# Optimization experiments

Hardware: AMD Instinct MI355X
Metric: run time of the kernel (lower is better)

Reference implementation:

```python
import jax, jax.numpy as jnp
import numpy as np

N_VARS = 28
HID = 64
BATCH = 32768
BN_EPS = 1e-5


def _lin_init(key, fan_in, shape):
    bound = 1.0 / np.sqrt(fan_in)
    return jax.random.uniform(key, shape, minval=-bound, maxval=bound, dtype=jnp.float32)


def setup_inputs() -> dict:
    key = jax.random.key(0)
    ks = jax.random.split(key, 8)
    n, h = N_VARS, HID
    X = jax.random.normal(ks[0], (BATCH, n), dtype=jnp.float32)
    W_logits = jax.random.uniform(ks[1], (n, n), minval=-0.01, maxval=0.01, dtype=jnp.float32)
    # per-mechanism (grouped) weights, stacked on leading mechanism axis n
    W1 = _lin_init(ks[2], n, (n, h, n)); b1 = _lin_init(ks[3], n, (n, h))
    W2 = _lin_init(ks[4], h, (n, h, h)); b2 = _lin_init(ks[5], h, (n, h))
    W3 = _lin_init(ks[6], h, (n, 1, h)); b3 = _lin_init(ks[7], h, (n, 1))
    gamma1 = jnp.ones((n, h)); beta1 = jnp.zeros((n, h))
    gamma2 = jnp.ones((n, h)); beta2 = jnp.zeros((n, h))
    return {"X": X, "W_logits": W_logits,
            "W1": W1, "b1": b1, "gamma1": gamma1, "beta1": beta1,
            "W2": W2, "b2": b2, "gamma2": gamma2, "beta2": beta2,
            "W3": W3, "b3": b3}


def _bn(x, gamma, beta):
    # x: [n, B, h]; batch stats over B (training-mode BatchNorm1d, biased var)
    m = x.mean(axis=1, keepdims=True)
    v = ((x - m) ** 2).mean(axis=1, keepdims=True)
    return gamma[:, None, :] * (x - m) * jax.lax.rsqrt(v + BN_EPS) + beta[:, None, :]


def reference(X, W_logits, W1, b1, gamma1, beta1, W2, b2, gamma2, beta2, W3, b3):
    n = W_logits.shape[0]
    # adjacency: sigmoid with zeroed diagonal
    W = jax.nn.sigmoid(W_logits) * (1.0 - jnp.eye(n, dtype=W_logits.dtype))
    # fuse the parent mask into the first layer's weights: one grouped GEMM
    # instead of n_vars separate masked matmuls
    W1_eff = W1 * W[:, None, :]                               # [n, h, n]
    h1 = jnp.einsum('bd,nhd->nbh', X, W1_eff) + b1[:, None, :]  # [n, B, h]
    a1 = jax.nn.gelu(_bn(h1, gamma1, beta1), approximate=False)
    h2 = jnp.einsum('nbh,ngh->nbg', a1, W2) + b2[:, None, :]
    a2 = jax.nn.gelu(_bn(h2, gamma2, beta2), approximate=False)
    out = jnp.einsum('nbh,noh->nbo', a2, W3) + b3[:, None, :]   # [n, B, 1]
    X_hat = out[:, :, 0].T                                     # [B, n]
    return (X_hat, W)
```

## Files before the change

kernel.cpp:

```cpp
#include <hip/hip_runtime.h>
#include <hip/hip_bf16.h>
#include <math.h>

typedef float  f4 __attribute__((ext_vector_type(4)));
typedef short  s8 __attribute__((ext_vector_type(8)));
typedef int    i2 __attribute__((ext_vector_type(2)));

#define NV 28
#define NB 32768
#define BN_EPS 1e-5f
#define NSLOT 434
#define PBLK 64

#define SUM2_OFF   0
#define SSQ2_OFF   1792
#define GATE_OFF   5376
#define PART_OFF   9472
#define BF_BASE_F  120640
#define XBF_OFF_S  172032
#define H2_BYTE_OFF 2924544ull
#define H2_BYTES    117440512ull

#define SMEM_BYTES 35840

__device__ __forceinline__ float gelu_f(float x) {
    float x2 = x * x;
    float z  = x * __builtin_fmaf(x2, -0.10294324f, -2.3022082f);
    float t  = __builtin_amdgcn_exp2f(z);
    return x * __builtin_amdgcn_rcpf(1.0f + t);
}
__device__ __forceinline__ unsigned short f2bf(float x) {
    unsigned u = __builtin_bit_cast(unsigned, x);
    return (unsigned short)((u + 0x7fffu + ((u >> 16) & 1u)) >> 16);
}
__device__ __forceinline__ int bfpack(float a, float b) {
    unsigned ua = __builtin_bit_cast(unsigned, a) + 0x8000u;
    unsigned ub = __builtin_bit_cast(unsigned, b) + 0x8000u;
    return __builtin_amdgcn_perm(ub, ua, 0x07060302);
}
__device__ __forceinline__ float row16_sum(float v) {
    int x;
    x = __builtin_amdgcn_update_dpp(0, __builtin_bit_cast(int, v), 0xB1, 0xF, 0xF, true);
    v += __builtin_bit_cast(float, x);
    x = __builtin_amdgcn_update_dpp(0, __builtin_bit_cast(int, v), 0x4E, 0xF, 0xF, true);
    v += __builtin_bit_cast(float, x);
    x = __builtin_amdgcn_update_dpp(0, __builtin_bit_cast(int, v), 0x124, 0xF, 0xF, true);
    v += __builtin_bit_cast(float, x);
    x = __builtin_amdgcn_update_dpp(0, __builtin_bit_cast(int, v), 0x128, 0xF, 0xF, true);
    v += __builtin_bit_cast(float, x);
    return v;
}
__device__ __forceinline__ float quad4_sum(float v) {
    int x;
    x = __builtin_amdgcn_update_dpp(0, __builtin_bit_cast(int, v), 0xB1, 0xF, 0xF, true);
    v += __builtin_bit_cast(float, x);
    x = __builtin_amdgcn_update_dpp(0, __builtin_bit_cast(int, v), 0x4E, 0xF, 0xF, true);
    v += __builtin_bit_cast(float, x);
    return v;
}
__device__ __forceinline__ void slot_de(int s, int& d, int& e) {
    int p = s - 28, dd = 0, rem = 28;
    while (p >= rem) { p -= rem; ++dd; --rem; }
    d = dd; e = dd + p;
}

__global__ __launch_bounds__(256) void k_prep(const float* __restrict__ X,
                                              const float* __restrict__ Wlog,
                                              float* __restrict__ ws,
                                              float* __restrict__ out) {
    __shared__ float sx[128 * 28];
    const int b = blockIdx.x, tid = threadIdx.x;
    if (b == PBLK) {
        for (int i = tid; i < 3584; i += 256) ws[SUM2_OFF + i] = 0.0f;
        unsigned* gates = (unsigned*)(ws + GATE_OFF);
        for (int i = tid; i < 28 * 32; i += 256) gates[i] = 0u;
        for (int i = tid; i < 784; i += 256) {
            float w = 1.0f / (1.0f + expf(-Wlog[i]));
            if ((i / 28) == (i % 28)) w = 0.0f;
            out[917504 + i] = w;
        }
        return;
    }
    const int s0 = tid;
    int d0 = 0, e0 = 0;
    if (s0 >= 28) slot_de(s0, d0, e0);
    const int s1 = tid + 256;
    const bool h1v = (s1 < NSLOT);
    int d1 = 0, e1 = 0;
    if (h1v) slot_de(s1, d1, e1);

    float a0 = 0.0f, a1 = 0.0f;
    int* xb = (int*)((short*)(ws + BF_BASE_F) + XBF_OFF_S);
#pragma unroll 1
    for (int ss = 0; ss < 4; ++ss) {
        const int rowbase = b * 512 + ss * 128;
        __syncthreads();
        {
            const f4* src = (const f4*)(X + (size_t)rowbase * 28);
            f4* dst = (f4*)sx;
            for (int i = tid; i < 896; i += 256) dst[i] = src[i];
        }
        __syncthreads();
        for (int j = tid; j < 2048; j += 256) {
            int row = j >> 4, cc = j & 15;
            float lo = (2 * cc     < 28) ? sx[row * 28 + 2 * cc]     : 0.0f;
            float hi = (2 * cc + 1 < 28) ? sx[row * 28 + 2 * cc + 1] : 0.0f;
            xb[(size_t)(rowbase + row) * 16 + cc] = (int)f2bf(lo) | ((int)f2bf(hi) << 16);
        }
        if (s0 < 28) {
            for (int r = 0; r < 128; ++r) a0 += sx[r * 28 + s0];
        } else {
            for (int r = 0; r < 128; ++r)
                a0 = __builtin_fmaf(sx[r * 28 + d0], sx[r * 28 + e0], a0);
        }
        if (h1v) {
            for (int r = 0; r < 128; ++r)
                a1 = __builtin_fmaf(sx[r * 28 + d1], sx[r * 28 + e1], a1);
        }
    }
    ws[PART_OFF + b * NSLOT + s0] = a0;
    if (h1v) ws[PART_OFF + b * NSLOT + s1] = a1;
}

__device__ __forceinline__ void fold_local(char* smemc, const float* __restrict__ Wlog,
                                           const float* __restrict__ W1,
                                           const float* __restrict__ g1,
                                           const float* __restrict__ be1,
                                           const float* __restrict__ W2,
                                           const float* __restrict__ ws, int n) {
    short* sW1   = (short*)smemc;
    short* sW2   = (short*)(smemc + 5120);
    float* fb    = (float*)(smemc + 14336);
    float* sstat = fb;
    float* mu    = fb + 434;
    float* wrow  = fb + 462;
    float* C     = fb + 490;
    float* w1e_s = fb + 1274;
    float* sBias = (float*)(smemc + 34816);
    const int t = threadIdx.x;

    __syncthreads();
    for (int s = t; s < NSLOT; s += 256) {
        float a = 0.0f;
#pragma unroll 8
        for (int p = 0; p < PBLK; ++p) a += ws[PART_OFF + p * NSLOT + s];
        sstat[s] = a;
    }
#pragma unroll
    for (int k = 0; k < 2; ++k) {
        int i = t + k * 256;
        int r = i >> 3, c = i & 7;
        const float* src = W2 + (size_t)n * 4096 + r * 64 + c * 8;
        s8 pk;
#pragma unroll
        for (int j = 0; j < 8; ++j) pk[j] = (short)f2bf(src[j]);
        *(s8*)&sW2[r * 72 + c * 8] = pk;
    }
    __syncthreads();
    if (t < 28) {
        mu[t] = sstat[t] * (1.0f / 32768.0f);
        float w = 1.0f / (1.0f + expf(-Wlog[n * 28 + t]));
        if (t == n) w = 0.0f;
        wrow[t] = w;
    }
    __syncthreads();
    for (int i = t; i < 784; i += 256) {
        int d = i / 28, e = i % 28;
        int lo = d < e ? d : e, hi = d < e ? e : d;
        int idx = 28 + lo * 28 - (lo * (lo - 1)) / 2 + (hi - lo);
        C[i] = sstat[idx] * (1.0f / 32768.0f) - mu[d] * mu[e];
    }
    for (int i = t; i < 1792; i += 256)
        w1e_s[i] = W1[(size_t)n * 1792 + i] * wrow[i % 28];
    __syncthreads();

    const int h = t >> 2, j = t & 3;
    const float* we = &w1e_s[h * 28];
    float var_p = 0.0f, dot_p = 0.0f;
#pragma unroll
    for (int k = 0; k < 7; ++k) {
        int d = 7 * j + k;
        float inner = 0.0f;
#pragma unroll
        for (int e = 0; e < 28; ++e) inner = __builtin_fmaf(C[d * 28 + e], we[e], inner);
        float wd = we[d];
        var_p = __builtin_fmaf(inner, wd, var_p);
        dot_p = __builtin_fmaf(wd, mu[d], dot_p);
    }
    float var  = quad4_sum(var_p);
    float dotm = quad4_sum(dot_p);
    float scale = g1[n * 64 + h] * rsqrtf(fmaxf(var, 0.0f) + BN_EPS);
    if (j == 0) sBias[h] = be1[n * 64 + h] - dotm * scale;
    {
        s8 pk;
#pragma unroll
        for (int k = 0; k < 8; ++k) {
            int d = 8 * j + k;
            pk[k] = (short)f2bf(d < 28 ? we[d] * scale : 0.0f);
        }
        *(s8*)&sW1[h * 40 + 8 * j] = pk;
    }
    __syncthreads();
}

__device__ __forceinline__ void pass1_item(char* smemc, float* __restrict__ ws,
                                           short* __restrict__ h2buf, int item) {
    short* sW1 = (short*)smemc;
    short* sW2 = (short*)(smemc + 5120);
    short* sA1 = (short*)(smemc + 14336);
    float* sP1 = (float*)(smemc + 32768);
    float* sP2 = (float*)(smemc + 33792);
    float* sBias = (float*)(smemc + 34816);
    const int n = item >> 8;
    const int blk = item & 255;
    const int tid = threadIdx.x;
    const int wave = tid >> 6;
    const int lane = tid & 63;
    const int m = lane & 15;
    const int q = lane >> 4;

    const short* xbf = (const short*)(ws + BF_BASE_F) + XBF_OFF_S;

    __syncthreads();
    f4 biasv[4];
#pragma unroll
    for (int t = 0; t < 4; ++t) biasv[t] = *(const f4*)&sBias[16 * t + 4 * q];

    short* myA1a = &sA1[(wave * 2 + 0) * 16 * 72];
    short* myA1b = &sA1[(wave * 2 + 1) * 16 * 72];
    float s1[16], s2v[16];

    const int row0 = blk * 128 + wave * 32;
    s8 xfa = *(const s8*)&xbf[(size_t)(row0 + m) * 32 + 8 * q];
    s8 xfb = *(const s8*)&xbf[(size_t)(row0 + 16 + m) * 32 + 8 * q];

    f4 acc1a[4], acc1b[4];
#pragma unroll
    for (int t = 0; t < 4; ++t) {
        s8 wf = *(const s8*)&sW1[(16 * t + m) * 40 + q * 8];
        acc1a[t] = __builtin_amdgcn_mfma_f32_16x16x32_bf16(wf, xfa, (f4){0.f, 0.f, 0.f, 0.f}, 0, 0, 0);
        acc1b[t] = __builtin_amdgcn_mfma_f32_16x16x32_bf16(wf, xfb, (f4){0.f, 0.f, 0.f, 0.f}, 0, 0, 0);
    }
#pragma unroll
    for (int t = 0; t < 4; ++t) {
        float ga0 = gelu_f(acc1a[t][0] + biasv[t][0]);
        float ga1 = gelu_f(acc1a[t][1] + biasv[t][1]);
        float ga2 = gelu_f(acc1a[t][2] + biasv[t][2]);
        float ga3 = gelu_f(acc1a[t][3] + biasv[t][3]);
        float gb0 = gelu_f(acc1b[t][0] + biasv[t][0]);
        float gb1 = gelu_f(acc1b[t][1] + biasv[t][1]);
        float gb2 = gelu_f(acc1b[t][2] + biasv[t][2]);
        float gb3 = gelu_f(acc1b[t][3] + biasv[t][3]);
        i2 pa = (i2){bfpack(ga0, ga1), bfpack(ga2, ga3)};
        i2 pb = (i2){bfpack(gb0, gb1), bfpack(gb2, gb3)};
        *(i2*)&myA1a[m * 72 + 16 * t + 4 * q] = pa;
        *(i2*)&myA1b[m * 72 + 16 * t + 4 * q] = pb;
    }
    s8 af0a = *(const s8*)&myA1a[m * 72 + 8 * q];
    s8 af1a = *(const s8*)&myA1a[m * 72 + 32 + 8 * q];
    s8 af0b = *(const s8*)&myA1b[m * 72 + 8 * q];
    s8 af1b = *(const s8*)&myA1b[m * 72 + 32 + 8 * q];
    short* hpA = h2buf + ((size_t)n * NB + row0 + m) * 64;
    short* hpB = h2buf + ((size_t)n * NB + row0 + 16 + m) * 64;
#pragma unroll
    for (int u = 0; u < 4; ++u) {
        s8 w0 = *(const s8*)&sW2[(16 * u + m) * 72 + 8 * q];
        s8 w1 = *(const s8*)&sW2[(16 * u + m) * 72 + 32 + 8 * q];
        f4 aa = (f4){0.f, 0.f, 0.f, 0.f};
        f4 ab = (f4){0.f, 0.f, 0.f, 0.f};
        aa = __builtin_amdgcn_mfma_f32_16x16x32_bf16(w0, af0a, aa, 0, 0, 0);
        ab = __builtin_amdgcn_mfma_f32_16x16x32_bf16(w0, af0b, ab, 0, 0, 0);
        aa = __builtin_amdgcn_mfma_f32_16x16x32_bf16(w1, af1a, aa, 0, 0, 0);
        ab = __builtin_amdgcn_mfma_f32_16x16x32_bf16(w1, af1b, ab, 0, 0, 0);
        i2 ha = (i2){bfpack(aa[0], aa[1]), bfpack(aa[2], aa[3])};
        i2 hb = (i2){bfpack(ab[0], ab[1]), bfpack(ab[2], ab[3])};
        *(i2*)&hpA[16 * u + 4 * q] = ha;
        *(i2*)&hpB[16 * u + 4 * q] = hb;
#pragma unroll
        for (int r = 0; r < 4; ++r) {
            s1[u * 4 + r]  = aa[r] + ab[r];
            float sq = __builtin_fmaf(aa[r], aa[r], ab[r] * ab[r]);
            s2v[u * 4 + r] = sq;
        }
    }
#pragma unroll
    for (int u = 0; u < 4; ++u) {
#pragma unroll
        for (int r = 0; r < 4; ++r) {
            float t1 = row16_sum(s1[u * 4 + r]);
            float t2 = row16_sum(s2v[u * 4 + r]);
            if (m == 0) {
                sP1[wave * 64 + 16 * u + 4 * q + r] = t1;
                sP2[wave * 64 + 16 * u + 4 * q + r] = t2;
            }
        }
    }
    __syncthreads();
    if (tid < 64) {
        float a = sP1[tid] + sP1[64 + tid] + sP1[128 + tid] + sP1[192 + tid];
        float b = sP2[tid] + sP2[64 + tid] + sP2[128 + tid] + sP2[192 + tid];
        atomicAdd(&ws[SUM2_OFF + n * 64 + tid], a);
        atomicAdd(&ws[SSQ2_OFF + n * 64 + tid], b);
    }
}

template <bool GATED>
__device__ __forceinline__ void pass2_item(char* smemc, const float* __restrict__ g2,
                                           const float* __restrict__ be2,
                                           const float* __restrict__ W3,
                                           const float* __restrict__ b3,
                                           float* __restrict__ ws,
                                           const short* __restrict__ h2buf,
                                           float* __restrict__ out, int item,
                                           unsigned* gates) {
    float* sSc  = (float*)(smemc + 35072);
    float* sSh  = (float*)(smemc + 35328);
    float* sW3v = (float*)(smemc + 35584);
    const int n = item >> 8;
    const int rbase = (item & 255) * 128;
    const int tid = threadIdx.x;
    if (GATED && tid == 0) {
        while (__hip_atomic_load(&gates[n * 32], __ATOMIC_RELAXED, __HIP_MEMORY_SCOPE_AGENT) < 256u)
            __builtin_amdgcn_s_sleep(2);
    }
    __syncthreads();
    if (tid < 64) {
        float su, sq;
        if (GATED) {
            su = __hip_atomic_load(&ws[SUM2_OFF + n * 64 + tid], __ATOMIC_RELAXED, __HIP_MEMORY_SCOPE_AGENT);
            sq = __hip_atomic_load(&ws[SSQ2_OFF + n * 64 + tid], __ATOMIC_RELAXED, __HIP_MEMORY_SCOPE_AGENT);
        } else {
            su = ws[SUM2_OFF + n * 64 + tid];
            sq = ws[SSQ2_OFF + n * 64 + tid];
        }
        float mean = su * (1.0f / 32768.0f);
        float var  = sq * (1.0f / 32768.0f) - mean * mean;
        float sc = g2[n * 64 + tid] * rsqrtf(fmaxf(var, 0.0f) + BN_EPS);
        sSc[tid]  = sc;
        sSh[tid]  = be2[n * 64 + tid] - mean * sc;
        sW3v[tid] = W3[n * 64 + tid];
    }
    __syncthreads();
    const int wave = tid >> 6;
    const int lane = tid & 63;
    const int rr = lane >> 3;
    const int cc = lane & 7;
    f4 scA = *(const f4*)&sSc[cc * 8],  scB = *(const f4*)&sSc[cc * 8 + 4];
    f4 shA = *(const f4*)&sSh[cc * 8],  shB = *(const f4*)&sSh[cc * 8 + 4];
    f4 w3A = *(const f4*)&sW3v[cc * 8], w3B = *(const f4*)&sW3v[cc * 8 + 4];
    const float b3n = b3[n];
#pragma unroll
    for (int it = 0; it < 4; ++it) {
        const int row = rbase + wave * 32 + it * 8 + rr;
        s8 hv = *(const s8*)(h2buf + ((size_t)n * NB + row) * 64 + cc * 8);
        float p = 0.0f;
#pragma unroll
        for (int j = 0; j < 4; ++j) {
            float v = __builtin_fmaf(__builtin_bit_cast(float, ((int)(unsigned short)hv[j]) << 16), scA[j], shA[j]);
            p = __builtin_fmaf(gelu_f(v), w3A[j], p);
        }
#pragma unroll
        for (int j = 0; j < 4; ++j) {
            float v = __builtin_fmaf(__builtin_bit_cast(float, ((int)(unsigned short)hv[4 + j]) << 16), scB[j], shB[j]);
            p = __builtin_fmaf(gelu_f(v), w3B[j], p);
        }
        p += __shfl_xor(p, 1);
        p += __shfl_xor(p, 2);
        p += __shfl_xor(p, 4);
        if (cc == 0) out[(size_t)row * 28 + n] = p + b3n;
    }
}

__global__ __launch_bounds__(256, 4) void k_mainG(const float* __restrict__ Wlog,
                                                  const float* __restrict__ W1,
                                                  const float* __restrict__ g1,
                                                  const float* __restrict__ be1,
                                                  const float* __restrict__ W2,
                                                  const float* __restrict__ g2,
                                                  const float* __restrict__ be2,
                                                  const float* __restrict__ W3,
                                                  const float* __restrict__ b3,
                                                  float* __restrict__ ws,
                                                  short* __restrict__ h2buf,
                                                  float* __restrict__ out) {
    __shared__ __align__(16) char smem[SMEM_BYTES];
    unsigned* gates = (unsigned*)(ws + GATE_OFF);
    const int b = blockIdx.x;
    const int tid = threadIdx.x;
    const int i0 = 7 * b;

    int cur = -1;
#pragma unroll 1
    for (int k = 0; k < 7; ++k) {
        const int item = i0 + k;
        const int n = item >> 8;
        if (n != cur) { fold_local(smem, Wlog, W1, g1, be1, W2, ws, n); cur = n; }
        pass1_item(smem, ws, h2buf, item);
        __syncthreads();
        if (tid == 0)
            __hip_atomic_fetch_add(&gates[n * 32], 1u, __ATOMIC_RELAXED, __HIP_MEMORY_SCOPE_AGENT);
    }
#pragma unroll 1
    for (int k = 0; k < 7; ++k)
        pass2_item<true>(smem, g2, be2, W3, b3, ws, h2buf, out, i0 + k, gates);
}

__global__ __launch_bounds__(256, 4) void kf_p1(const float* __restrict__ Wlog,
                                                const float* __restrict__ W1,
                                                const float* __restrict__ g1,
                                                const float* __restrict__ be1,
                                                const float* __restrict__ W2,
                                                float* __restrict__ ws,
                                                short* __restrict__ h2buf) {
    __shared__ __align__(16) char smem[SMEM_BYTES];
    const int i0 = 7 * blockIdx.x;
    int cur = -1;
#pragma unroll 1
    for (int k = 0; k < 7; ++k) {
        const int item = i0 + k;
        const int n = item >> 8;
        if (n != cur) { fold_local(smem, Wlog, W1, g1, be1, W2, ws, n); cur = n; }
        pass1_item(smem, ws, h2buf, item);
    }
}
__global__ __launch_bounds__(256, 4) void kf_p2(const float* __restrict__ g2,
                                                const float* __restrict__ be2,
                                                const float* __restrict__ W3,
                                                const float* __restrict__ b3,
                                                float* __restrict__ ws,
                                                const short* __restrict__ h2buf,
                                                float* __restrict__ out) {
    __shared__ __align__(16) char smem[SMEM_BYTES];
    const int i0 = 7 * blockIdx.x;
#pragma unroll 1
    for (int k = 0; k < 7; ++k)
        pass2_item<false>(smem, g2, be2, W3, b3, ws, h2buf, out, i0 + k, nullptr);
}

extern "C" void kernel_launch(void* const* d_in, const int* in_sizes, int n_in,
                              void* d_out, int out_size, void* d_ws, size_t ws_size,
                              hipStream_t stream) {
    const float* X   = (const float*)d_in[0];
    const float* Wl  = (const float*)d_in[1];
    const float* W1  = (const float*)d_in[2];
    const float* g1  = (const float*)d_in[4];
    const float* be1 = (const float*)d_in[5];
    const float* W2  = (const float*)d_in[6];
    const float* g2  = (const float*)d_in[8];
    const float* be2 = (const float*)d_in[9];
    const float* W3  = (const float*)d_in[10];
    const float* b3  = (const float*)d_in[11];
    float* out = (float*)d_out;
    float* ws  = (float*)d_ws;
    short* h2buf = (short*)((char*)d_ws + H2_BYTE_OFF);

    static int gmain = 0;
    if (gmain == 0) {
        int dev = 0;
        hipDeviceProp_t prop;
        bool ok = (hipGetDevice(&dev) == hipSuccess) &&
                  (hipGetDeviceProperties(&prop, dev) == hipSuccess) &&
                  prop.cooperativeLaunch;
        int bpc = 0;
        if (ok &&
            hipOccupancyMaxActiveBlocksPerMultiprocessor(&bpc, k_mainG, 256, 0) == hipSuccess &&
            (long)bpc * prop.multiProcessorCount >= 1024) {
            gmain = 1;
        } else {
            gmain = -1;
        }
    }

    k_prep<<<dim3(PBLK + 1), dim3(256), 0, stream>>>(X, Wl, ws, out);

    bool done = false;
    if (gmain > 0) {
        void* args[12] = {(void*)&Wl, (void*)&W1, (void*)&g1, (void*)&be1, (void*)&W2,
                          (void*)&g2, (void*)&be2, (void*)&W3, (void*)&b3,
                          (void*)&ws, (void*)&h2buf, (void*)&out};
        hipError_t e = hipLaunchCooperativeKernel(reinterpret_cast<const void*>(k_mainG),
                                                  dim3(1024), dim3(256), args, 0, stream);
        if (e == hipSuccess) done = true;
        else gmain = -1;
    }
    if (!done) {
        kf_p1<<<dim3(1024), dim3(256), 0, stream>>>(Wl, W1, g1, be1, W2, ws, h2buf);
        kf_p2<<<dim3(1024), dim3(256), 0, stream>>>(g2, be2, W3, b3, ws, h2buf, out);
    }
}
```

Baseline: 203.2 us.

## Compute first-layer BN fold once per mechanism and share via global gates

The first-layer weight fold (covariance reduction, BN scale and bias, bf16 packing) used to be recomputed by every block for every mechanism it touched. It now runs once per mechanism in 28 designated blocks, which publish the folded W1 and bias to global memory and set a per-mechanism gate. The remaining blocks spin on that gate and copy the results into shared memory. W2 is converted to bf16 once in extra prep blocks instead of per block. This removes redundant fold work, but every block now has to wait for the 28 folding blocks before starting, which adds a dependency stall.

```diff
diff --git a/kernel.cpp b/kernel.cpp
--- a/kernel.cpp
+++ b/kernel.cpp
@@ -15,8 +15,11 @@
 #define SUM2_OFF   0
 #define SSQ2_OFF   1792
 #define GATE_OFF   5376
-#define PART_OFF   9472
+#define BIAS1_OFF  7424
+#define W1F_OFF    9216
+#define PART_OFF   37888
 #define BF_BASE_F  120640
+#define W2B_OFF_S  57344
 #define XBF_OFF_S  172032
 #define H2_BYTE_OFF 2924544ull
 #define H2_BYTES    117440512ull
@@ -66,6 +69,7 @@
 
 __global__ __launch_bounds__(256) void k_prep(const float* __restrict__ X,
                                               const float* __restrict__ Wlog,
+                                              const float* __restrict__ W2,
                                               float* __restrict__ ws,
                                               float* __restrict__ out) {
     __shared__ float sx[128 * 28];
@@ -73,12 +77,25 @@
     if (b == PBLK) {
         for (int i = tid; i < 3584; i += 256) ws[SUM2_OFF + i] = 0.0f;
         unsigned* gates = (unsigned*)(ws + GATE_OFF);
-        for (int i = tid; i < 28 * 32; i += 256) gates[i] = 0u;
+        for (int i = tid; i < 2048; i += 256) gates[i] = 0u;
         for (int i = tid; i < 784; i += 256) {
             float w = 1.0f / (1.0f + expf(-Wlog[i]));
             if ((i / 28) == (i % 28)) w = 0.0f;
             out[917504 + i] = w;
         }
+        return;
+    }
+    if (b > PBLK) {
+        const int n = b - PBLK - 1;
+        const float* w2src = W2 + (size_t)n * 4096 + tid * 16;
+        short* w2d = (short*)(ws + BF_BASE_F) + W2B_OFF_S + (size_t)n * 4096 + tid * 16;
+        s8 a, c;
+#pragma unroll
+        for (int k = 0; k < 8; ++k) a[k] = (short)f2bf(w2src[k]);
+#pragma unroll
+        for (int k = 0; k < 8; ++k) c[k] = (short)f2bf(w2src[8 + k]);
+        *(s8*)&w2d[0] = a;
+        *(s8*)&w2d[8] = c;
         return;
     }
     const int s0 = tid;
@@ -122,40 +139,25 @@
     if (h1v) ws[PART_OFF + b * NSLOT + s1] = a1;
 }
 
-__device__ __forceinline__ void fold_local(char* smemc, const float* __restrict__ Wlog,
-                                           const float* __restrict__ W1,
-                                           const float* __restrict__ g1,
-                                           const float* __restrict__ be1,
-                                           const float* __restrict__ W2,
-                                           const float* __restrict__ ws, int n) {
-    short* sW1   = (short*)smemc;
-    short* sW2   = (short*)(smemc + 5120);
+__device__ __forceinline__ void fold_global(char* smemc, const float* __restrict__ Wlog,
+                                            const float* __restrict__ W1,
+                                            const float* __restrict__ g1,
+                                            const float* __restrict__ be1,
+                                            float* __restrict__ ws, int n) {
     float* fb    = (float*)(smemc + 14336);
     float* sstat = fb;
     float* mu    = fb + 434;
     float* wrow  = fb + 462;
     float* C     = fb + 490;
     float* w1e_s = fb + 1274;
-    float* sBias = (float*)(smemc + 34816);
     const int t = threadIdx.x;
 
-    __syncthreads();
     for (int s = t; s < NSLOT; s += 256) {
         float a = 0.0f;
 #pragma unroll 8
         for (int p = 0; p < PBLK; ++p) a += ws[PART_OFF + p * NSLOT + s];
         sstat[s] = a;
     }
-#pragma unroll
-    for (int k = 0; k < 2; ++k) {
-        int i = t + k * 256;
-        int r = i >> 3, c = i & 7;
-        const float* src = W2 + (size_t)n * 4096 + r * 64 + c * 8;
-        s8 pk;
-#pragma unroll
-        for (int j = 0; j < 8; ++j) pk[j] = (short)f2bf(src[j]);
-        *(s8*)&sW2[r * 72 + c * 8] = pk;
-    }
     __syncthreads();
     if (t < 28) {
         mu[t] = sstat[t] * (1.0f / 32768.0f);
@@ -190,15 +192,56 @@
     float var  = quad4_sum(var_p);
     float dotm = quad4_sum(dot_p);
     float scale = g1[n * 64 + h] * rsqrtf(fmaxf(var, 0.0f) + BN_EPS);
-    if (j == 0) sBias[h] = be1[n * 64 + h] - dotm * scale;
-    {
-        s8 pk;
-#pragma unroll
-        for (int k = 0; k < 8; ++k) {
-            int d = 8 * j + k;
-            pk[k] = (short)f2bf(d < 28 ? we[d] * scale : 0.0f);
-        }
-        *(s8*)&sW1[h * 40 + 8 * j] = pk;
+    if (j == 0)
+        __hip_atomic_store(&ws[BIAS1_OFF + n * 64 + h], be1[n * 64 + h] - dotm * scale,
+                           __ATOMIC_RELAXED, __HIP_MEMORY_SCOPE_AGENT);
+    unsigned* w1f = (unsigned*)ws + W1F_OFF + n * 1024;
+#pragma unroll
+    for (int k = 0; k < 4; ++k) {
+        int d0 = 8 * j + 2 * k, d1 = d0 + 1;
+        unsigned lo = (unsigned)f2bf(d0 < 28 ? we[d0] * scale : 0.0f);
+        unsigned hi = (unsigned)f2bf(d1 < 28 ? we[d1] * scale : 0.0f);
+        __hip_atomic_store(&w1f[h * 16 + j * 4 + k], lo | (hi << 16),
+                           __ATOMIC_RELAXED, __HIP_MEMORY_SCOPE_AGENT);
+    }
+    __syncthreads();
+    if (t == 0)
+        __hip_atomic_store((unsigned*)(ws + GATE_OFF) + 896 + n * 32, 1u,
+                           __ATOMIC_RELAXED, __HIP_MEMORY_SCOPE_AGENT);
+}
+
+template <bool GATED>
+__device__ __forceinline__ void weights_stage(char* smemc, float* __restrict__ ws, int n) {
+    short* sW1   = (short*)smemc;
+    short* sW2   = (short*)(smemc + 5120);
+    float* sBias = (float*)(smemc + 34816);
+    const int tid = threadIdx.x;
+    __syncthreads();
+    if (GATED && tid == 0) {
+        unsigned* wg = (unsigned*)(ws + GATE_OFF) + 896 + n * 32;
+        while (__hip_atomic_load(wg, __ATOMIC_RELAXED, __HIP_MEMORY_SCOPE_AGENT) < 1u)
+            __builtin_amdgcn_s_sleep(2);
+    }
+    __syncthreads();
+    const unsigned* w1f = (const unsigned*)ws + W1F_OFF + n * 1024;
+#pragma unroll
+    for (int k = 0; k < 4; ++k) {
+        int i = tid + k * 256;
+        unsigned v = GATED ? __hip_atomic_load(&w1f[i], __ATOMIC_RELAXED, __HIP_MEMORY_SCOPE_AGENT)
+                           : w1f[i];
+        int r = i >> 4, c = i & 15;
+        *(unsigned*)((char*)sW1 + r * 80 + c * 4) = v;
+    }
+    if (tid < 64)
+        sBias[tid] = GATED ? __hip_atomic_load(&ws[BIAS1_OFF + n * 64 + tid],
+                                               __ATOMIC_RELAXED, __HIP_MEMORY_SCOPE_AGENT)
+                           : ws[BIAS1_OFF + n * 64 + tid];
+    const short* w2g = (const short*)(ws + BF_BASE_F) + W2B_OFF_S + (size_t)n * 4096;
+#pragma unroll
+    for (int k = 0; k < 2; ++k) {
+        int i = tid + k * 256;
+        int r = i >> 3, c = i & 7;
+        *(s8*)&sW2[r * 72 + c * 8] = *(const s8*)&w2g[r * 64 + c * 8];
     }
     __syncthreads();
 }
@@ -279,8 +322,7 @@
 #pragma unroll
         for (int r = 0; r < 4; ++r) {
             s1[u * 4 + r]  = aa[r] + ab[r];
-            float sq = __builtin_fmaf(aa[r], aa[r], ab[r] * ab[r]);
-            s2v[u * 4 + r] = sq;
+            s2v[u * 4 + r] = __builtin_fmaf(aa[r], aa[r], ab[r] * ab[r]);
         }
     }
 #pragma unroll
@@ -375,7 +417,6 @@
                                                   const float* __restrict__ W1,
                                                   const float* __restrict__ g1,
                                                   const float* __restrict__ be1,
-                                                  const float* __restrict__ W2,
                                                   const float* __restrict__ g2,
                                                   const float* __restrict__ be2,
                                                   const float* __restrict__ W3,
@@ -389,12 +430,14 @@
     const int tid = threadIdx.x;
     const int i0 = 7 * b;
 
+    if (b < 28) fold_global(smem, Wlog, W1, g1, be1, ws, b);
+
     int cur = -1;
 #pragma unroll 1
     for (int k = 0; k < 7; ++k) {
         const int item = i0 + k;
         const int n = item >> 8;
-        if (n != cur) { fold_local(smem, Wlog, W1, g1, be1, W2, ws, n); cur = n; }
+        if (n != cur) { weights_stage<true>(smem, ws, n); cur = n; }
         pass1_item(smem, ws, h2buf, item);
         __syncthreads();
         if (tid == 0)
@@ -405,12 +448,15 @@
         pass2_item<true>(smem, g2, be2, W3, b3, ws, h2buf, out, i0 + k, gates);
 }
 
-__global__ __launch_bounds__(256, 4) void kf_p1(const float* __restrict__ Wlog,
-                                                const float* __restrict__ W1,
-                                                const float* __restrict__ g1,
-                                                const float* __restrict__ be1,
-                                                const float* __restrict__ W2,
-                                                float* __restrict__ ws,
+__global__ __launch_bounds__(256) void kf_fold(const float* __restrict__ Wlog,
+                                               const float* __restrict__ W1,
+                                               const float* __restrict__ g1,
+                                               const float* __restrict__ be1,
+                                               float* __restrict__ ws) {
+    __shared__ __align__(16) char smem[SMEM_BYTES];
+    fold_global(smem, Wlog, W1, g1, be1, ws, blockIdx.x);
+}
+__global__ __launch_bounds__(256, 4) void kf_p1(float* __restrict__ ws,
                                                 short* __restrict__ h2buf) {
     __shared__ __align__(16) char smem[SMEM_BYTES];
     const int i0 = 7 * blockIdx.x;
@@ -419,7 +465,7 @@
     for (int k = 0; k < 7; ++k) {
         const int item = i0 + k;
         const int n = item >> 8;
-        if (n != cur) { fold_local(smem, Wlog, W1, g1, be1, W2, ws, n); cur = n; }
+        if (n != cur) { weights_stage<false>(smem, ws, n); cur = n; }
         pass1_item(smem, ws, h2buf, item);
     }
 }
@@ -471,11 +517,11 @@
         }
     }
 
-    k_prep<<<dim3(PBLK + 1), dim3(256), 0, stream>>>(X, Wl, ws, out);
+    k_prep<<<dim3(PBLK + 1 + 28), dim3(256), 0, stream>>>(X, Wl, W2, ws, out);
 
     bool done = false;
     if (gmain > 0) {
-        void* args[12] = {(void*)&Wl, (void*)&W1, (void*)&g1, (void*)&be1, (void*)&W2,
+        void* args[11] = {(void*)&Wl, (void*)&W1, (void*)&g1, (void*)&be1,
                           (void*)&g2, (void*)&be2, (void*)&W3, (void*)&b3,
                           (void*)&ws, (void*)&h2buf, (void*)&out};
         hipError_t e = hipLaunchCooperativeKernel(reinterpret_cast<const void*>(k_mainG),
@@ -484,7 +530,8 @@
         else gmain = -1;
     }
     if (!done) {
-        kf_p1<<<dim3(1024), dim3(256), 0, stream>>>(Wl, W1, g1, be1, W2, ws, h2buf);
-        kf_p2<<<dim3(1024), dim3(256), 0, stream>>>(g2, be2, W3, b3, ws, h2buf, out);
-    }
-}
+        kf_fold<<<dim3(28),   dim3(256), 0, stream>>>(Wl, W1, g1, be1, ws);
+        kf_p1  <<<dim3(1024), dim3(256), 0, stream>>>(ws, h2buf);
+        kf_p2  <<<dim3(1024), dim3(256), 0, stream>>>(g2, be2, W3, b3, ws, h2buf, out);
+    }
+}
```

Result: faster. 194.7 us (-4.2%).

## Replace cooperative gated kernel with three plain launches and precomputed bf16 W2

Applied to the files above, without the earlier changes.

Removes the cooperative single-kernel path, whose blocks spin on per-mechanism gate counters between pass 1 and pass 2, and replaces it with three ordinary launches: prep, pass 1 and pass 2. Pass 1 now uses 896 blocks, each bound to one mechanism so the BN1 fold runs once per block. Pass 2 becomes a fine-grained kernel with one 128-row tile per block. The bf16 conversion of W2 moves into extra prep blocks so each pass-1 block copies pre-converted weights. This trades the gate spin-waits and the cooperative launch for an extra kernel boundary and more, smaller pass-2 blocks.

```diff
diff --git a/kernel.cpp b/kernel.cpp
--- a/kernel.cpp
+++ b/kernel.cpp
@@ -14,14 +14,14 @@
 
 #define SUM2_OFF   0
 #define SSQ2_OFF   1792
-#define GATE_OFF   5376
 #define PART_OFF   9472
 #define BF_BASE_F  120640
+#define W2B_OFF_S  57344
 #define XBF_OFF_S  172032
 #define H2_BYTE_OFF 2924544ull
 #define H2_BYTES    117440512ull
 
-#define SMEM_BYTES 35840
+#define SMEM_BYTES 35072
 
 __device__ __forceinline__ float gelu_f(float x) {
     float x2 = x * x;
@@ -66,19 +66,31 @@
 
 __global__ __launch_bounds__(256) void k_prep(const float* __restrict__ X,
                                               const float* __restrict__ Wlog,
+                                              const float* __restrict__ W2,
                                               float* __restrict__ ws,
                                               float* __restrict__ out) {
     __shared__ float sx[128 * 28];
     const int b = blockIdx.x, tid = threadIdx.x;
     if (b == PBLK) {
         for (int i = tid; i < 3584; i += 256) ws[SUM2_OFF + i] = 0.0f;
-        unsigned* gates = (unsigned*)(ws + GATE_OFF);
-        for (int i = tid; i < 28 * 32; i += 256) gates[i] = 0u;
         for (int i = tid; i < 784; i += 256) {
             float w = 1.0f / (1.0f + expf(-Wlog[i]));
             if ((i / 28) == (i % 28)) w = 0.0f;
             out[917504 + i] = w;
         }
+        return;
+    }
+    if (b > PBLK) {
+        const int n = b - PBLK - 1;
+        const float* w2src = W2 + (size_t)n * 4096 + tid * 16;
+        short* w2d = (short*)(ws + BF_BASE_F) + W2B_OFF_S + (size_t)n * 4096 + tid * 16;
+        s8 a, c;
+#pragma unroll
+        for (int k = 0; k < 8; ++k) a[k] = (short)f2bf(w2src[k]);
+#pragma unroll
+        for (int k = 0; k < 8; ++k) c[k] = (short)f2bf(w2src[8 + k]);
+        *(s8*)&w2d[0] = a;
+        *(s8*)&w2d[8] = c;
         return;
     }
     const int s0 = tid;
@@ -126,7 +138,6 @@
                                            const float* __restrict__ W1,
                                            const float* __restrict__ g1,
                                            const float* __restrict__ be1,
-                                           const float* __restrict__ W2,
                                            const float* __restrict__ ws, int n) {
     short* sW1   = (short*)smemc;
     short* sW2   = (short*)(smemc + 5120);
@@ -139,22 +150,18 @@
     float* sBias = (float*)(smemc + 34816);
     const int t = threadIdx.x;
 
-    __syncthreads();
     for (int s = t; s < NSLOT; s += 256) {
         float a = 0.0f;
 #pragma unroll 8
         for (int p = 0; p < PBLK; ++p) a += ws[PART_OFF + p * NSLOT + s];
         sstat[s] = a;
     }
+    const short* w2g = (const short*)(ws + BF_BASE_F) + W2B_OFF_S + (size_t)n * 4096;
 #pragma unroll
     for (int k = 0; k < 2; ++k) {
         int i = t + k * 256;
         int r = i >> 3, c = i & 7;
-        const float* src = W2 + (size_t)n * 4096 + r * 64 + c * 8;
-        s8 pk;
-#pragma unroll
-        for (int j = 0; j < 8; ++j) pk[j] = (short)f2bf(src[j]);
-        *(s8*)&sW2[r * 72 + c * 8] = pk;
+        *(s8*)&sW2[r * 72 + c * 8] = *(const s8*)&w2g[r * 64 + c * 8];
     }
     __syncthreads();
     if (t < 28) {
@@ -279,8 +286,7 @@
 #pragma unroll
         for (int r = 0; r < 4; ++r) {
             s1[u * 4 + r]  = aa[r] + ab[r];
-            float sq = __builtin_fmaf(aa[r], aa[r], ab[r] * ab[r]);
-            s2v[u * 4 + r] = sq;
+            s2v[u * 4 + r] = __builtin_fmaf(aa[r], aa[r], ab[r] * ab[r]);
         }
     }
 #pragma unroll
@@ -304,37 +310,36 @@
     }
 }
 
-template <bool GATED>
-__device__ __forceinline__ void pass2_item(char* smemc, const float* __restrict__ g2,
-                                           const float* __restrict__ be2,
-                                           const float* __restrict__ W3,
-                                           const float* __restrict__ b3,
-                                           float* __restrict__ ws,
-                                           const short* __restrict__ h2buf,
-                                           float* __restrict__ out, int item,
-                                           unsigned* gates) {
-    float* sSc  = (float*)(smemc + 35072);
-    float* sSh  = (float*)(smemc + 35328);
-    float* sW3v = (float*)(smemc + 35584);
-    const int n = item >> 8;
-    const int rbase = (item & 255) * 128;
+__global__ __launch_bounds__(256, 4) void k_p1f(const float* __restrict__ Wlog,
+                                                const float* __restrict__ W1,
+                                                const float* __restrict__ g1,
+                                                const float* __restrict__ be1,
+                                                float* __restrict__ ws,
+                                                short* __restrict__ h2buf) {
+    __shared__ __align__(16) char smem[SMEM_BYTES];
+    const int b = blockIdx.x;
+    const int n = b >> 5;
+    const int sub = b & 31;
+    fold_local(smem, Wlog, W1, g1, be1, ws, n);
+#pragma unroll 1
+    for (int k = 0; k < 8; ++k)
+        pass1_item(smem, ws, h2buf, (n << 8) + sub * 8 + k);
+}
+
+__global__ __launch_bounds__(256) void k_pass2c(const float* __restrict__ g2,
+                                                const float* __restrict__ be2,
+                                                const float* __restrict__ W3,
+                                                const float* __restrict__ b3,
+                                                const float* __restrict__ ws,
+                                                const short* __restrict__ h2buf,
+                                                float* __restrict__ out) {
+    __shared__ float sSc[64], sSh[64], sW3v[64];
+    const int n = blockIdx.x >> 8;
+    const int rbase = (blockIdx.x & 255) * 128;
     const int tid = threadIdx.x;
-    if (GATED && tid == 0) {
-        while (__hip_atomic_load(&gates[n * 32], __ATOMIC_RELAXED, __HIP_MEMORY_SCOPE_AGENT) < 256u)
-            __builtin_amdgcn_s_sleep(2);
-    }
-    __syncthreads();
     if (tid < 64) {
-        float su, sq;
-        if (GATED) {
-            su = __hip_atomic_load(&ws[SUM2_OFF + n * 64 + tid], __ATOMIC_RELAXED, __HIP_MEMORY_SCOPE_AGENT);
-            sq = __hip_atomic_load(&ws[SSQ2_OFF + n * 64 + tid], __ATOMIC_RELAXED, __HIP_MEMORY_SCOPE_AGENT);
-        } else {
-            su = ws[SUM2_OFF + n * 64 + tid];
-            sq = ws[SSQ2_OFF + n * 64 + tid];
-        }
-        float mean = su * (1.0f / 32768.0f);
-        float var  = sq * (1.0f / 32768.0f) - mean * mean;
+        float mean = ws[SUM2_OFF + n * 64 + tid] * (1.0f / 32768.0f);
+        float var  = ws[SSQ2_OFF + n * 64 + tid] * (1.0f / 32768.0f) - mean * mean;
         float sc = g2[n * 64 + tid] * rsqrtf(fmaxf(var, 0.0f) + BN_EPS);
         sSc[tid]  = sc;
         sSh[tid]  = be2[n * 64 + tid] - mean * sc;
@@ -369,72 +374,6 @@
         p += __shfl_xor(p, 4);
         if (cc == 0) out[(size_t)row * 28 + n] = p + b3n;
     }
-}
-
-__global__ __launch_bounds__(256, 4) void k_mainG(const float* __restrict__ Wlog,
-                                                  const float* __restrict__ W1,
-                                                  const float* __restrict__ g1,
-                                                  const float* __restrict__ be1,
-                                                  const float* __restrict__ W2,
-                                                  const float* __restrict__ g2,
-                                                  const float* __restrict__ be2,
-                                                  const float* __restrict__ W3,
-                                                  const float* __restrict__ b3,
-                                                  float* __restrict__ ws,
-                                                  short* __restrict__ h2buf,
-                                                  float* __restrict__ out) {
-    __shared__ __align__(16) char smem[SMEM_BYTES];
-    unsigned* gates = (unsigned*)(ws + GATE_OFF);
-    const int b = blockIdx.x;
-    const int tid = threadIdx.x;
-    const int i0 = 7 * b;
-
-    int cur = -1;
-#pragma unroll 1
-    for (int k = 0; k < 7; ++k) {
-        const int item = i0 + k;
-        const int n = item >> 8;
-        if (n != cur) { fold_local(smem, Wlog, W1, g1, be1, W2, ws, n); cur = n; }
-        pass1_item(smem, ws, h2buf, item);
-        __syncthreads();
-        if (tid == 0)
-            __hip_atomic_fetch_add(&gates[n * 32], 1u, __ATOMIC_RELAXED, __HIP_MEMORY_SCOPE_AGENT);
-    }
-#pragma unroll 1
-    for (int k = 0; k < 7; ++k)
-        pass2_item<true>(smem, g2, be2, W3, b3, ws, h2buf, out, i0 + k, gates);
-}
-
-__global__ __launch_bounds__(256, 4) void kf_p1(const float* __restrict__ Wlog,
-                                                const float* __restrict__ W1,
-                                                const float* __restrict__ g1,
-                                                const float* __restrict__ be1,
-                                                const float* __restrict__ W2,
-                                                float* __restrict__ ws,
-                                                short* __restrict__ h2buf) {
-    __shared__ __align__(16) char smem[SMEM_BYTES];
-    const int i0 = 7 * blockIdx.x;
-    int cur = -1;
-#pragma unroll 1
-    for (int k = 0; k < 7; ++k) {
-        const int item = i0 + k;
-        const int n = item >> 8;
-        if (n != cur) { fold_local(smem, Wlog, W1, g1, be1, W2, ws, n); cur = n; }
-        pass1_item(smem, ws, h2buf, item);
-    }
-}
-__global__ __launch_bounds__(256, 4) void kf_p2(const float* __restrict__ g2,
-                                                const float* __restrict__ be2,
-                                                const float* __restrict__ W3,
-                                                const float* __restrict__ b3,
-                                                float* __restrict__ ws,
-                                                const short* __restrict__ h2buf,
-                                                float* __restrict__ out) {
-    __shared__ __align__(16) char smem[SMEM_BYTES];
-    const int i0 = 7 * blockIdx.x;
-#pragma unroll 1
-    for (int k = 0; k < 7; ++k)
-        pass2_item<false>(smem, g2, be2, W3, b3, ws, h2buf, out, i0 + k, nullptr);
 }
 
 extern "C" void kernel_launch(void* const* d_in, const int* in_sizes, int n_in,
@@ -454,37 +393,7 @@
     float* ws  = (float*)d_ws;
     short* h2buf = (short*)((char*)d_ws + H2_BYTE_OFF);
 
-    static int gmain = 0;
-    if (gmain == 0) {
-        int dev = 0;
-        hipDeviceProp_t prop;
-        bool ok = (hipGetDevice(&dev) == hipSuccess) &&
-                  (hipGetDeviceProperties(&prop, dev) == hipSuccess) &&
-                  prop.cooperativeLaunch;
-        int bpc = 0;
-        if (ok &&
-            hipOccupancyMaxActiveBlocksPerMultiprocessor(&bpc, k_mainG, 256, 0) == hipSuccess &&
-            (long)bpc * prop.multiProcessorCount >= 1024) {
-            gmain = 1;
-        } else {
-            gmain = -1;
-        }
-    }
-
-    k_prep<<<dim3(PBLK + 1), dim3(256), 0, stream>>>(X, Wl, ws, out);
-
-    bool done = false;
-    if (gmain > 0) {
-        void* args[12] = {(void*)&Wl, (void*)&W1, (void*)&g1, (void*)&be1, (void*)&W2,
-                          (void*)&g2, (void*)&be2, (void*)&W3, (void*)&b3,
-                          (void*)&ws, (void*)&h2buf, (void*)&out};
-        hipError_t e = hipLaunchCooperativeKernel(reinterpret_cast<const void*>(k_mainG),
-                                                  dim3(1024), dim3(256), args, 0, stream);
-        if (e == hipSuccess) done = true;
-        else gmain = -1;
-    }
-    if (!done) {
-        kf_p1<<<dim3(1024), dim3(256), 0, stream>>>(Wl, W1, g1, be1, W2, ws, h2buf);
-        kf_p2<<<dim3(1024), dim3(256), 0, stream>>>(g2, be2, W3, b3, ws, h2buf, out);
-    }
-}
+    k_prep  <<<dim3(PBLK + 1 + 28), dim3(256), 0, stream>>>(X, Wl, W2, ws, out);
+    k_p1f   <<<dim3(896),           dim3(256), 0, stream>>>(Wl, W1, g1, be1, ws, h2buf);
+    k_pass2c<<<dim3(28 * 256),      dim3(256), 0, stream>>>(g2, be2, W3, b3, ws, h2buf, out);
+}
```

Result: faster. 193.5 us (-4.8%).
